# Kernel optimization log

Hardware: AMD Instinct MI355X
Metric: run time of the kernel (lower is better)

The kernel has to match this reference:

```python
import jax, jax.numpy as jnp
import numpy as np

# ---- static CRF config (mirrors label_vocab / __init__) ----
LABEL_VOCAB = {"O": 0}
for _i in range(25):
    LABEL_VOCAB["B-T%d" % _i] = 1 + 2 * _i
    LABEL_VOCAB["I-T%d" % _i] = 2 + 2 * _i
NUM_LABELS = len(LABEL_VOCAB)          # 51
LABEL_SIZE = NUM_LABELS + 2            # 53
START = LABEL_SIZE - 2                 # 51
END = LABEL_SIZE - 1                   # 52
BIOES = False


def _init_transition(raw):
    """Replicates CRF.initialize() on a randn (L, L) matrix. axis0=to, axis1=from."""
    t = np.asarray(raw, dtype=np.float32).copy()
    t[:, END] = -100.0
    t[START, :] = 100.0
    for label, idx in LABEL_VOCAB.items():
        if label.startswith('I-') or label.endswith('E-'):
            t[idx, START] = -100.0
        if label.startswith('B-') or label.endswith('I-'):
            t[END, idx] = 100.0
    for lf, fi in LABEL_VOCAB.items():
        fp, ft = ('O', 'O') if lf == 'O' else tuple(lf.split('-', 1))
        for lt, ti in LABEL_VOCAB.items():
            tp, tt = ('O', 'O') if lt == 'O' else tuple(lt.split('-', 1))
            if BIOES:
                allowed = (fp in ['O', 'E', 'S'] and tp in ['O', 'B', 'S']) or (
                    fp in ['B', 'I'] and tp in ['I', 'E'] and ft == tt)
            else:
                allowed = (tp in ['B', 'O']) or (
                    fp in ['B', 'O'] and tp == 'I' and ft == tt)
            if not allowed:
                t[ti, fi] = -100.0
    return jnp.asarray(t)


def setup_inputs() -> dict:
    key = jax.random.key(0)
    k1, k2, k3, k4 = jax.random.split(key, 4)
    B, S = 256, 2048
    logits = jax.random.normal(k1, (B, S, NUM_LABELS), dtype=jnp.float32)
    labels = jax.random.randint(k2, (B, S), 0, NUM_LABELS).astype(jnp.int64)
    lens = jax.random.randint(k3, (B,), 1, S).astype(jnp.int64)
    transition = _init_transition(jax.random.normal(k4, (LABEL_SIZE, LABEL_SIZE)))
    return {"logits": logits, "labels": labels, "lens": lens, "transition": transition}


def reference(logits, labels, lens, transition):
    """CRF.loglik = gold_score - norm_score, returns (batch,)."""
    B, S, _ = logits.shape
    dt = logits.dtype
    # pad_logits: append two -100 columns for start/end
    logits_p = jnp.concatenate(
        [logits, jnp.full((B, S, 2), -100.0, dt)], axis=2)  # (B, S, LABEL_SIZE)

    # ---- unary (emission) score ----
    mask_s = (jnp.arange(S)[None, :] < lens[:, None]).astype(dt)       # (B, S)
    unary = jnp.take_along_axis(logits_p, labels[:, :, None], axis=2)[..., 0]
    unary = jnp.sum(unary * mask_s, axis=1)                            # (B,)

    # ---- binary (transition) score ----
    lab_ext = jnp.concatenate(
        [jnp.full((B, 1), START, labels.dtype), labels,
         jnp.full((B, 1), END, labels.dtype)], axis=1)                 # (B, S+2)
    mask_e = jnp.arange(S + 2)[None, :] < (lens + 1)[:, None]
    lab_ext = jnp.where(mask_e, lab_ext, END)
    to_l = lab_ext[:, 1:]                                              # (B, S+1)
    fr_l = lab_ext[:, :-1]
    trn_scr = transition[to_l, fr_l]                                   # (B, S+1)
    mask_b = (jnp.arange(S + 1)[None, :] < (lens + 1)[:, None]).astype(dt)
    binary = jnp.sum(trn_scr * mask_b, axis=1)                         # (B,)
    gold = unary + binary

    # ---- partition function (forward algorithm, sequential logsumexp) ----
    alpha0 = jnp.full((B, LABEL_SIZE), -100.0, dt).at[:, START].set(0.0)
    logits_t = jnp.transpose(logits_p, (1, 0, 2))                      # (S, B, L)

    def step(alpha, inp):
        logit, t = inp                                                 # (B, L), scalar
        # mat[b, to, fr] = alpha[b, fr] + trans[to, fr] + logit[b, to]
        mat = alpha[:, None, :] + transition[None, :, :] + logit[:, :, None]
        alpha_nxt = jax.scipy.special.logsumexp(mat, axis=2)           # (B, L)
        keep = (t < lens)[:, None]
        return jnp.where(keep, alpha_nxt, alpha), None

    alpha, _ = jax.lax.scan(step, alpha0, (logits_t, jnp.arange(S)))
    norm = jax.scipy.special.logsumexp(alpha + transition[END][None, :], axis=1)
    return gold - norm
```

## Files before the change

### kernel.cpp

```cpp
#include <hip/hip_runtime.h>

#define S_LEN 2048
#define NL 51
#define LS 53
#define ST 51
#define EN 52
#define NBATCH 256
#define L2E 1.4426950408889634f
#define LN2 0.6931471805599453f

typedef float f32x4 __attribute__((ext_vector_type(4)));

__device__ __forceinline__ float rlane(float v, int l) {
    return __builtin_bit_cast(float, __builtin_amdgcn_readlane(__builtin_bit_cast(int, v), l));
}

__global__ __launch_bounds__(192, 1) void crf_kernel(
    const float* __restrict__ logits,
    const int*   __restrict__ labels,
    const int*   __restrict__ lens,
    const float* __restrict__ Tr,
    float*       __restrict__ out)
{
    const int b   = blockIdx.x;
    const int tid = threadIdx.x;
    const int len = lens[b];
    const int bsteps = len >> 1;
    const int fsteps = len - bsteps;

    __shared__ float sh_gold;
    __shared__ float sh_eb[64];
    __shared__ float sh_off2b;

    const float* lg = logits + (long)b * S_LEN * NL;

    float eF = 0.f, off2F = 0.f;

#define RL4(G) float b##G##0 = rlane(e, 4*G), b##G##1 = rlane(e, 4*G+1), \
                     b##G##2 = rlane(e, 4*G+2), b##G##3 = rlane(e, 4*G+3);
#define FM4(G, EV) { ax = fmaf(b##G##0, EV.x, ax); ay = fmaf(b##G##1, EV.y, ay); \
                     az = fmaf(b##G##2, EV.z, az); aw = fmaf(b##G##3, EV.w, aw); }
#define MATVEC(SOUT) { \
            RL4(0) RL4(1) RL4(2) RL4(3) RL4(4) RL4(5) RL4(6) \
            RL4(7) RL4(8) RL4(9) RL4(10) RL4(11) RL4(12) \
            float b130 = rlane(e, 52); \
            __builtin_amdgcn_sched_barrier(0); \
            float ax = 0.f, ay = 0.f, az = 0.f, aw = 0.f; \
            FM4(0, er0) FM4(1, er1) FM4(2, er2) FM4(3, er3) FM4(4, er4) \
            FM4(5, er5) FM4(6, er6) FM4(7, er7) FM4(8, er8) FM4(9, er9) \
            FM4(10, er10) FM4(11, er11) FM4(12, er12) \
            ax = fmaf(b130, er13.x, ax); \
            SOUT = (ax + ay) + (az + aw); }
#define STEP(NLV, DL, MV) { \
            float sv; MATVEC(sv); \
            e = sv * q; \
            float ssum = rlane(sv, DL); \
            off2 += lprev; \
            lprev = __builtin_amdgcn_logf(ssum); \
            float nl = (lane < NL) ? (NLV) : (MV); \
            q = __builtin_amdgcn_exp2f((nl + tmax) * L2E) * __builtin_amdgcn_rcpf(ssum); }

    if (tid >= 128) {
        const int lid = tid - 128;
        const int* lb = labels + (long)b * S_LEN;
        float p = 0.f;
        for (int t = lid; t < len; t += 64) {
            const int lab  = lb[t];
            const int prev = (t == 0) ? ST : lb[t - 1];
            p += lg[(long)t * NL + lab] + Tr[lab * LS + prev];
        }
        if (lid == 0) p += Tr[EN * LS + lb[len - 1]];
#pragma unroll
        for (int off = 32; off > 0; off >>= 1)
            p += __shfl_down(p, off, 64);
        if (lid == 0) sh_gold = p;
    } else if (tid >= 64) {
        const int lane = tid - 64;
        const int jj = (lane < NL) ? lane : 0;

        f32x4 er0, er1, er2, er3, er4, er5, er6, er7, er8, er9, er10, er11, er12, er13;
#define GTB(K) (((lane < LS) && ((K) < LS)) ? \
                (Tr[(K) * LS + lane] - ((((K)==ST)||((K)==EN)) ? 100.f : 0.f)) : -1e30f)
#define LD4B(V,B) { V.x = GTB(B); V.y = GTB((B)+1); V.z = GTB((B)+2); V.w = GTB((B)+3); }
        LD4B(er0, 0)  LD4B(er1, 4)  LD4B(er2, 8)   LD4B(er3, 12)
        LD4B(er4, 16) LD4B(er5, 20) LD4B(er6, 24)  LD4B(er7, 28)
        LD4B(er8, 32) LD4B(er9, 36) LD4B(er10, 40) LD4B(er11, 44)
        LD4B(er12, 48) LD4B(er13, 52)
#undef GTB
#undef LD4B
        float tmax = -1e30f;
#define MX4(V) tmax = fmaxf(tmax, fmaxf(fmaxf(V.x, V.y), fmaxf(V.z, V.w)));
        MX4(er0) MX4(er1) MX4(er2) MX4(er3) MX4(er4) MX4(er5) MX4(er6)
        MX4(er7) MX4(er8) MX4(er9) MX4(er10) MX4(er11) MX4(er12) MX4(er13)
#undef MX4
#define EX4(V) { V.x = __builtin_amdgcn_exp2f((V.x - tmax) * L2E); \
                 V.y = __builtin_amdgcn_exp2f((V.y - tmax) * L2E); \
                 V.z = __builtin_amdgcn_exp2f((V.z - tmax) * L2E); \
                 V.w = __builtin_amdgcn_exp2f((V.w - tmax) * L2E); }
        EX4(er0) EX4(er1) EX4(er2) EX4(er3) EX4(er4) EX4(er5) EX4(er6)
        EX4(er7) EX4(er8) EX4(er9) EX4(er10) EX4(er11) EX4(er12) EX4(er13)
#undef EX4

        float rawEN = (lane < LS) ? (Tr[EN * LS + lane] - 100.f) : -1e30f;
        float e     = __builtin_amdgcn_exp2f(rawEN * L2E);
        float off2  = 100.f * L2E;
        float lprev = 0.f;
        float q     = __builtin_amdgcn_exp2f(tmax * L2E);

        float buf[4] = {0.f, 0.f, 0.f, 0.f};
        if (bsteps >= 1) {
            float nlL = (lane < NL) ? lg[(long)(len - 1) * NL + jj] : 0.f;
            e *= __builtin_amdgcn_exp2f(nlL * L2E);
            int r;
            buf[0] = lg[(long)(len - 2) * NL + jj];
            r = len - 3; r = r < 0 ? 0 : r; buf[1] = lg[(long)r * NL + jj];
            r = len - 4; r = r < 0 ? 0 : r; buf[2] = lg[(long)r * NL + jj];
            r = len - 5; r = r < 0 ? 0 : r; buf[3] = lg[(long)r * NL + jj];
        }

        int i = 0;
#pragma unroll 1
        while (i + 4 <= bsteps) {
            { int pr = len - 6 - i; pr = pr < 0 ? 0 : pr;
              float pf = lg[(long)pr * NL + jj]; STEP(buf[0], 53, 0.f) buf[0] = pf; }
            { int pr = len - 7 - i; pr = pr < 0 ? 0 : pr;
              float pf = lg[(long)pr * NL + jj]; STEP(buf[1], 53, 0.f) buf[1] = pf; }
            { int pr = len - 8 - i; pr = pr < 0 ? 0 : pr;
              float pf = lg[(long)pr * NL + jj]; STEP(buf[2], 53, 0.f) buf[2] = pf; }
            { int pr = len - 9 - i; pr = pr < 0 ? 0 : pr;
              float pf = lg[(long)pr * NL + jj]; STEP(buf[3], 53, 0.f) buf[3] = pf; }
            i += 4;
        }
#pragma unroll
        for (int m = 0; m < 4; ++m) {
            if (i + m < bsteps) { STEP(buf[m], 53, 0.f) }
        }

        sh_eb[lane] = e;
        if (lane == 0) sh_off2b = off2;
    } else {
        const int lane = tid;
        const int jj = (lane < NL) ? lane : 0;
        const float* trow = Tr + lane * LS;

        f32x4 er0, er1, er2, er3, er4, er5, er6, er7, er8, er9, er10, er11, er12, er13;
#define GT(K)    (((lane < LS) && ((K) < LS)) ? trow[(K)] : -1e30f)
#define LD4(V,B) { V.x = GT(B); V.y = GT((B)+1); V.z = GT((B)+2); V.w = GT((B)+3); }
        LD4(er0, 0)  LD4(er1, 4)  LD4(er2, 8)   LD4(er3, 12)
        LD4(er4, 16) LD4(er5, 20) LD4(er6, 24)  LD4(er7, 28)
        LD4(er8, 32) LD4(er9, 36) LD4(er10, 40) LD4(er11, 44)
        LD4(er12, 48) LD4(er13, 52)
#undef GT
#undef LD4
        float tmax = -1e30f;
#define MX4(V) tmax = fmaxf(tmax, fmaxf(fmaxf(V.x, V.y), fmaxf(V.z, V.w)));
        MX4(er0) MX4(er1) MX4(er2) MX4(er3) MX4(er4) MX4(er5) MX4(er6)
        MX4(er7) MX4(er8) MX4(er9) MX4(er10) MX4(er11) MX4(er12) MX4(er13)
#undef MX4
#define EX4(V) { V.x = __builtin_amdgcn_exp2f((V.x - tmax) * L2E); \
                 V.y = __builtin_amdgcn_exp2f((V.y - tmax) * L2E); \
                 V.z = __builtin_amdgcn_exp2f((V.z - tmax) * L2E); \
                 V.w = __builtin_amdgcn_exp2f((V.w - tmax) * L2E); }
        EX4(er0) EX4(er1) EX4(er2) EX4(er3) EX4(er4) EX4(er5) EX4(er6)
        EX4(er7) EX4(er8) EX4(er9) EX4(er10) EX4(er11) EX4(er12) EX4(er13)
#undef EX4

        float buf[4];
        buf[0] = lg[0 * NL + jj];
        buf[1] = lg[1 * NL + jj];
        buf[2] = lg[2 * NL + jj];
        buf[3] = lg[3 * NL + jj];

        float e     = (lane == ST) ? 1.f : 0.f;
        float off2  = 0.f;
        float lprev = 0.f;
        float nl0   = (lane < NL) ? buf[0] : -100.f;
        float q     = __builtin_amdgcn_exp2f((nl0 + tmax) * L2E);

        int t = 0;
#pragma unroll 1
        while (t + 4 <= fsteps) {
            {
                float pf = lg[(long)(t + 4) * NL + jj];
                STEP(buf[1], ST, -100.f)
                buf[0] = pf;
            }
            {
                int ti = t + 5; ti = (ti < S_LEN) ? ti : (S_LEN - 1);
                float pf = lg[(long)ti * NL + jj];
                STEP(buf[2], ST, -100.f)
                buf[1] = pf;
            }
            {
                int ti = t + 6; ti = (ti < S_LEN) ? ti : (S_LEN - 1);
                float pf = lg[(long)ti * NL + jj];
                STEP(buf[3], ST, -100.f)
                buf[2] = pf;
            }
            {
                int ti = t + 7; ti = (ti < S_LEN) ? ti : (S_LEN - 1);
                float pf = lg[(long)ti * NL + jj];
                STEP(buf[0], ST, -100.f)
                buf[3] = pf;
            }
            t += 4;
        }
#pragma unroll
        for (int i = 0; i < 4; ++i) {
            if (t + i < fsteps) {
                STEP(buf[(i + 1) & 3], ST, -100.f)
            }
        }

        eF    = e;
        off2F = off2;
    }
#undef STEP
#undef MATVEC
#undef RL4
#undef FM4

    __syncthreads();

    if (tid < 64) {
        float d = eF * sh_eb[tid];
#pragma unroll
        for (int off = 32; off > 0; off >>= 1)
            d += __shfl_xor(d, off, 64);
        if (tid == 0) {
            float norm = LN2 * (off2F + sh_off2b + __builtin_amdgcn_logf(d));
            out[b] = sh_gold - norm;
        }
    }
}

extern "C" void kernel_launch(void* const* d_in, const int* in_sizes, int n_in,
                              void* d_out, int out_size, void* d_ws, size_t ws_size,
                              hipStream_t stream) {
    const float* logits = (const float*)d_in[0];
    const int*   labels = (const int*)d_in[1];
    const int*   lens   = (const int*)d_in[2];
    const float* Tr     = (const float*)d_in[3];
    float*       out    = (float*)d_out;
    crf_kernel<<<NBATCH, 192, 0, stream>>>(logits, labels, lens, Tr, out);
}
```

Baseline: 356.8 us.

## Replace readlane broadcast in matvec with DPP/permlane swizzled register layout

The per-step 53x53 matvec used 53 scalar readlanes to broadcast alpha values across the wave. It now uses permlane32/16 swaps plus DPP quad-perm and row-mirror moves to build 64 lane-permuted copies of e, and the transition matrix is stored in a matching XOR-swizzled register layout. The aim is to take the readlane/SGPR serialization off the sequential critical path. In exchange it does 64 multiply-adds instead of 53 and adds DPP latency and register pressure.

```diff
diff --git a/kernel.cpp b/kernel.cpp
--- a/kernel.cpp
+++ b/kernel.cpp
@@ -10,10 +10,13 @@
 #define LN2 0.6931471805599453f
 
 typedef float f32x4 __attribute__((ext_vector_type(4)));
+typedef unsigned int u32x2 __attribute__((ext_vector_type(2)));
 
 __device__ __forceinline__ float rlane(float v, int l) {
     return __builtin_bit_cast(float, __builtin_amdgcn_readlane(__builtin_bit_cast(int, v), l));
 }
+
+#define DPP(SRC, CTRL) __builtin_amdgcn_update_dpp(0, (SRC), (CTRL), 0xF, 0xF, false)
 
 __global__ __launch_bounds__(192, 1) void crf_kernel(
     const float* __restrict__ logits,
@@ -36,29 +39,77 @@
 
     float eF = 0.f, off2F = 0.f;
 
-#define RL4(G) float b##G##0 = rlane(e, 4*G), b##G##1 = rlane(e, 4*G+1), \
-                     b##G##2 = rlane(e, 4*G+2), b##G##3 = rlane(e, 4*G+3);
-#define FM4(G, EV) { ax = fmaf(b##G##0, EV.x, ax); ay = fmaf(b##G##1, EV.y, ay); \
-                     az = fmaf(b##G##2, EV.z, az); aw = fmaf(b##G##3, EV.w, aw); }
+#define PALL(M) M(0,0) M(0,1) M(0,2) M(0,3) M(1,0) M(1,1) M(1,2) M(1,3) \
+                M(2,0) M(2,1) M(2,2) M(2,3) M(3,0) M(3,1) M(3,2) M(3,3)
+#define DECLP(B,G) f32x4 p##B##_##G;
+#define LDP(B,G,GETTER) { \
+        p##B##_##G.x = GETTER((((lane ^ (4*(G)+0)) & 15) + 16*(B))); \
+        p##B##_##G.y = GETTER((((lane ^ (4*(G)+1)) & 15) + 16*(B))); \
+        p##B##_##G.z = GETTER((((lane ^ (4*(G)+2)) & 15) + 16*(B))); \
+        p##B##_##G.w = GETTER((((lane ^ (4*(G)+3)) & 15) + 16*(B))); }
+#define MAXP(B,G) tmax = fmaxf(tmax, \
+        fmaxf(fmaxf(p##B##_##G.x, p##B##_##G.y), fmaxf(p##B##_##G.z, p##B##_##G.w)));
+#define EXPP(B,G) { \
+        p##B##_##G.x = __builtin_amdgcn_exp2f((p##B##_##G.x - tmax) * L2E); \
+        p##B##_##G.y = __builtin_amdgcn_exp2f((p##B##_##G.y - tmax) * L2E); \
+        p##B##_##G.z = __builtin_amdgcn_exp2f((p##B##_##G.z - tmax) * L2E); \
+        p##B##_##G.w = __builtin_amdgcn_exp2f((p##B##_##G.w - tmax) * L2E); }
+#define PINP(B,G) asm volatile("" : "+v"(p##B##_##G));
+
+#define BQ(B) \
+        const int r##B##_1 = DPP(r##B##_0, 177); \
+        const int r##B##_2 = DPP(r##B##_0, 78);  \
+        const int r##B##_3 = DPP(r##B##_0, 27);
+#define BH(B) \
+        const int r##B##_7 = DPP(r##B##_0, 0x141); \
+        const int r##B##_6 = DPP(r##B##_1, 0x141); \
+        const int r##B##_5 = DPP(r##B##_2, 0x141); \
+        const int r##B##_4 = DPP(r##B##_3, 0x141);
+#define BMIR(B) \
+        const int r##B##_15 = DPP(r##B##_0, 0x140); \
+        const int r##B##_14 = DPP(r##B##_1, 0x140); \
+        const int r##B##_13 = DPP(r##B##_2, 0x140); \
+        const int r##B##_12 = DPP(r##B##_3, 0x140); \
+        const int r##B##_11 = DPP(r##B##_4, 0x140); \
+        const int r##B##_10 = DPP(r##B##_5, 0x140); \
+        const int r##B##_9  = DPP(r##B##_6, 0x140); \
+        const int r##B##_8  = DPP(r##B##_7, 0x140);
+#define BCAST \
+        const int e_i = __builtin_bit_cast(int, e); \
+        const u32x2 sw32 = __builtin_amdgcn_permlane32_swap((unsigned)e_i, (unsigned)e_i, false, false); \
+        const u32x2 swA  = __builtin_amdgcn_permlane16_swap(sw32[0], sw32[0], false, false); \
+        const u32x2 swB  = __builtin_amdgcn_permlane16_swap(sw32[1], sw32[1], false, false); \
+        const int r0_0 = (int)swA[0]; const int r1_0 = (int)swA[1]; \
+        const int r2_0 = (int)swB[0]; const int r3_0 = (int)swB[1]; \
+        BQ(0) BQ(1) BQ(2) BQ(3) \
+        BH(0) BH(1) BH(2) BH(3) \
+        BMIR(0) BMIR(1) BMIR(2) BMIR(3)
+
+#define RF(B,X) __builtin_bit_cast(float, r##B##_##X)
+#define FB8L(B) { \
+        aL##B = fmaf(RF(B,0),  p##B##_0.x, aL##B); aH##B = fmaf(RF(B,1),  p##B##_0.y, aH##B); \
+        aL##B = fmaf(RF(B,2),  p##B##_0.z, aL##B); aH##B = fmaf(RF(B,3),  p##B##_0.w, aH##B); \
+        aL##B = fmaf(RF(B,4),  p##B##_1.x, aL##B); aH##B = fmaf(RF(B,5),  p##B##_1.y, aH##B); \
+        aL##B = fmaf(RF(B,6),  p##B##_1.z, aL##B); aH##B = fmaf(RF(B,7),  p##B##_1.w, aH##B); }
+#define FB8H(B) { \
+        aL##B = fmaf(RF(B,8),  p##B##_2.x, aL##B); aH##B = fmaf(RF(B,9),  p##B##_2.y, aH##B); \
+        aL##B = fmaf(RF(B,10), p##B##_2.z, aL##B); aH##B = fmaf(RF(B,11), p##B##_2.w, aH##B); \
+        aL##B = fmaf(RF(B,12), p##B##_3.x, aL##B); aH##B = fmaf(RF(B,13), p##B##_3.y, aH##B); \
+        aL##B = fmaf(RF(B,14), p##B##_3.z, aL##B); aH##B = fmaf(RF(B,15), p##B##_3.w, aH##B); }
 #define MATVEC(SOUT) { \
-            RL4(0) RL4(1) RL4(2) RL4(3) RL4(4) RL4(5) RL4(6) \
-            RL4(7) RL4(8) RL4(9) RL4(10) RL4(11) RL4(12) \
-            float b130 = rlane(e, 52); \
-            __builtin_amdgcn_sched_barrier(0); \
-            float ax = 0.f, ay = 0.f, az = 0.f, aw = 0.f; \
-            FM4(0, er0) FM4(1, er1) FM4(2, er2) FM4(3, er3) FM4(4, er4) \
-            FM4(5, er5) FM4(6, er6) FM4(7, er7) FM4(8, er8) FM4(9, er9) \
-            FM4(10, er10) FM4(11, er11) FM4(12, er12) \
-            ax = fmaf(b130, er13.x, ax); \
-            SOUT = (ax + ay) + (az + aw); }
+        float aL0=0.f,aH0=0.f,aL1=0.f,aH1=0.f,aL2=0.f,aH2=0.f,aL3=0.f,aH3=0.f; \
+        FB8L(0) FB8H(0) FB8L(1) FB8H(1) FB8L(2) FB8H(2) FB8L(3) FB8H(3) \
+        SOUT = ((aL0+aH0)+(aL1+aH1)) + ((aL2+aH2)+(aL3+aH3)); }
+
 #define STEP(NLV, DL, MV) { \
-            float sv; MATVEC(sv); \
-            e = sv * q; \
-            float ssum = rlane(sv, DL); \
-            off2 += lprev; \
-            lprev = __builtin_amdgcn_logf(ssum); \
-            float nl = (lane < NL) ? (NLV) : (MV); \
-            q = __builtin_amdgcn_exp2f((nl + tmax) * L2E) * __builtin_amdgcn_rcpf(ssum); }
+        BCAST \
+        float sv; MATVEC(sv) \
+        e = sv * q; \
+        const float ssum = rlane(sv, DL); \
+        off2 += lprev; \
+        lprev = __builtin_amdgcn_logf(ssum); \
+        const float nl = (lane < NL) ? (NLV) : (MV); \
+        q = __builtin_amdgcn_exp2f((nl + tmax) * L2E) * __builtin_amdgcn_rcpf(ssum); }
 
     if (tid >= 128) {
         const int lid = tid - 128;
@@ -78,28 +129,17 @@
         const int lane = tid - 64;
         const int jj = (lane < NL) ? lane : 0;
 
-        f32x4 er0, er1, er2, er3, er4, er5, er6, er7, er8, er9, er10, er11, er12, er13;
-#define GTB(K) (((lane < LS) && ((K) < LS)) ? \
-                (Tr[(K) * LS + lane] - ((((K)==ST)||((K)==EN)) ? 100.f : 0.f)) : -1e30f)
-#define LD4B(V,B) { V.x = GTB(B); V.y = GTB((B)+1); V.z = GTB((B)+2); V.w = GTB((B)+3); }
-        LD4B(er0, 0)  LD4B(er1, 4)  LD4B(er2, 8)   LD4B(er3, 12)
-        LD4B(er4, 16) LD4B(er5, 20) LD4B(er6, 24)  LD4B(er7, 28)
-        LD4B(er8, 32) LD4B(er9, 36) LD4B(er10, 40) LD4B(er11, 44)
-        LD4B(er12, 48) LD4B(er13, 52)
+        PALL(DECLP)
+#define GTB(C) (((lane < LS) && ((C) < LS)) ? \
+                (Tr[(C) * LS + lane] - ((((C)==ST)||((C)==EN)) ? 100.f : 0.f)) : -1e30f)
+#define LDPB(B,G) LDP(B,G,GTB)
+        PALL(LDPB)
+#undef LDPB
+        float tmax = -1e30f;
+        PALL(MAXP)
+        PALL(EXPP)
+        PALL(PINP)
 #undef GTB
-#undef LD4B
-        float tmax = -1e30f;
-#define MX4(V) tmax = fmaxf(tmax, fmaxf(fmaxf(V.x, V.y), fmaxf(V.z, V.w)));
-        MX4(er0) MX4(er1) MX4(er2) MX4(er3) MX4(er4) MX4(er5) MX4(er6)
-        MX4(er7) MX4(er8) MX4(er9) MX4(er10) MX4(er11) MX4(er12) MX4(er13)
-#undef MX4
-#define EX4(V) { V.x = __builtin_amdgcn_exp2f((V.x - tmax) * L2E); \
-                 V.y = __builtin_amdgcn_exp2f((V.y - tmax) * L2E); \
-                 V.z = __builtin_amdgcn_exp2f((V.z - tmax) * L2E); \
-                 V.w = __builtin_amdgcn_exp2f((V.w - tmax) * L2E); }
-        EX4(er0) EX4(er1) EX4(er2) EX4(er3) EX4(er4) EX4(er5) EX4(er6)
-        EX4(er7) EX4(er8) EX4(er9) EX4(er10) EX4(er11) EX4(er12) EX4(er13)
-#undef EX4
 
         float rawEN = (lane < LS) ? (Tr[EN * LS + lane] - 100.f) : -1e30f;
         float e     = __builtin_amdgcn_exp2f(rawEN * L2E);
@@ -143,27 +183,16 @@
         const int jj = (lane < NL) ? lane : 0;
         const float* trow = Tr + lane * LS;
 
-        f32x4 er0, er1, er2, er3, er4, er5, er6, er7, er8, er9, er10, er11, er12, er13;
-#define GT(K)    (((lane < LS) && ((K) < LS)) ? trow[(K)] : -1e30f)
-#define LD4(V,B) { V.x = GT(B); V.y = GT((B)+1); V.z = GT((B)+2); V.w = GT((B)+3); }
-        LD4(er0, 0)  LD4(er1, 4)  LD4(er2, 8)   LD4(er3, 12)
-        LD4(er4, 16) LD4(er5, 20) LD4(er6, 24)  LD4(er7, 28)
-        LD4(er8, 32) LD4(er9, 36) LD4(er10, 40) LD4(er11, 44)
-        LD4(er12, 48) LD4(er13, 52)
-#undef GT
-#undef LD4
+        PALL(DECLP)
+#define GTF(C) (((lane < LS) && ((C) < LS)) ? trow[(C)] : -1e30f)
+#define LDPF(B,G) LDP(B,G,GTF)
+        PALL(LDPF)
+#undef LDPF
         float tmax = -1e30f;
-#define MX4(V) tmax = fmaxf(tmax, fmaxf(fmaxf(V.x, V.y), fmaxf(V.z, V.w)));
-        MX4(er0) MX4(er1) MX4(er2) MX4(er3) MX4(er4) MX4(er5) MX4(er6)
-        MX4(er7) MX4(er8) MX4(er9) MX4(er10) MX4(er11) MX4(er12) MX4(er13)
-#undef MX4
-#define EX4(V) { V.x = __builtin_amdgcn_exp2f((V.x - tmax) * L2E); \
-                 V.y = __builtin_amdgcn_exp2f((V.y - tmax) * L2E); \
-                 V.z = __builtin_amdgcn_exp2f((V.z - tmax) * L2E); \
-                 V.w = __builtin_amdgcn_exp2f((V.w - tmax) * L2E); }
-        EX4(er0) EX4(er1) EX4(er2) EX4(er3) EX4(er4) EX4(er5) EX4(er6)
-        EX4(er7) EX4(er8) EX4(er9) EX4(er10) EX4(er11) EX4(er12) EX4(er13)
-#undef EX4
+        PALL(MAXP)
+        PALL(EXPP)
+        PALL(PINP)
+#undef GTF
 
         float buf[4];
         buf[0] = lg[0 * NL + jj];
@@ -215,10 +244,6 @@
         eF    = e;
         off2F = off2;
     }
-#undef STEP
-#undef MATVEC
-#undef RL4
-#undef FM4
 
     __syncthreads();
 
```

Measured after the change: 547.5 us. +53.5%, slower.
